# Kernel optimization log

Hardware: AMD Instinct MI355X
Metric: run time of the kernel (lower is better)

## Reference

```python
import jax, jax.numpy as jnp
import numpy as np
import math

N_NODES = 50000
N_EDGES = 800000
D_IN = 128
HID = 128  # layer dims: 128 -> 128 -> 64 -> 32


def _glorot(key, fan_in, fan_out):
    lim = math.sqrt(6.0 / (fan_in + fan_out))
    return jax.random.uniform(key, (fan_in, fan_out), jnp.float32, -lim, lim)


def setup_inputs() -> dict:
    key = jax.random.key(0)
    ks = jax.random.split(key, 9)
    x = jax.random.normal(ks[0], (N_NODES, D_IN), dtype=jnp.float32)
    edge_index = jax.random.randint(ks[1], (2, N_EDGES), 0, N_NODES, dtype=jnp.int64)
    edge_attr = jax.random.uniform(ks[2], (N_EDGES,), dtype=jnp.float32)
    return {
        "x": x,
        "edge_index": edge_index,
        "edge_attr": edge_attr,
        "W1": _glorot(ks[3], D_IN, HID),      "b1": jnp.zeros((HID,), jnp.float32),
        "W2": _glorot(ks[4], HID, HID // 2),  "b2": jnp.zeros((HID // 2,), jnp.float32),
        "W3": _glorot(ks[5], HID // 2, HID // 4), "b3": jnp.zeros((HID // 4,), jnp.float32),
    }


def _gcn_conv(h, W, b, src, dst, norm, n_nodes):
    # GCNConv: linear transform, then normalized scatter-add aggregation, then bias
    h = h @ W                                   # [N, F_out]
    msg = h[src] * norm[:, None]                # gather + scale, [E', F_out]
    out = jax.ops.segment_sum(msg, dst, num_segments=n_nodes)  # scatter-add
    return out + b


def reference(x, edge_index, edge_attr, W1, b1, W2, b2, W3, b3):
    n = x.shape[0]
    # add self-loops with weight 1.0 (PyG GCNConv default)
    loop = jnp.arange(n, dtype=edge_index.dtype)
    src = jnp.concatenate([edge_index[0], loop])
    dst = jnp.concatenate([edge_index[1], loop])
    w = jnp.concatenate([edge_attr, jnp.ones((n,), edge_attr.dtype)])
    # symmetric normalization: D^{-1/2} A_hat D^{-1/2}
    deg = jax.ops.segment_sum(w, dst, num_segments=n)
    dinv = jnp.where(deg > 0, jax.lax.rsqrt(jnp.maximum(deg, 1e-30)), 0.0)
    norm = dinv[src] * w * dinv[dst]            # [E + N]

    h = jax.nn.relu(_gcn_conv(x, W1, b1, src, dst, norm, n))
    # dropout is identity in eval mode
    h = jax.nn.relu(_gcn_conv(h, W2, b2, src, dst, norm, n))
    h = _gcn_conv(h, W3, b3, src, dst, norm, n)
    return h
```

## Files before the change

kernel.cpp:

```cpp
#include <hip/hip_runtime.h>
#include <hip/hip_bf16.h>

#define BLK 256
#define SCAT_NB 512
#define BIN_SHIFT 8

typedef unsigned short ushort_t;
typedef unsigned int uint_t;
typedef unsigned long long ull_t;
typedef __attribute__((ext_vector_type(8))) short bf16x8;
typedef __attribute__((ext_vector_type(4))) float f32x4;

static __device__ __forceinline__ float bf2f(ushort_t u) {
    return __uint_as_float((uint_t)u << 16);
}
static __device__ __forceinline__ ushort_t f2bf(float f) {
    __hip_bfloat16 h = __float2bfloat16(f);
    return *reinterpret_cast<ushort_t*>(&h);
}


__global__ __launch_bounds__(256) void k_pre(const int* __restrict__ eidx,
                                             int* __restrict__ bcnt,
                                             int nbins, int epb, int E,
                                             const float* __restrict__ x,
                                             ushort_t* __restrict__ xb, int n4,
                                             const float* __restrict__ W1, ushort_t* __restrict__ Wt1,
                                             const float* __restrict__ W2, ushort_t* __restrict__ Wt2,
                                             const float* __restrict__ W3, ushort_t* __restrict__ Wt3) {
    const int b = blockIdx.x;
    const int t = threadIdx.x;
    if (b < SCAT_NB) {
        __shared__ int h[256];
        h[t] = 0;
        __syncthreads();
        const int base = b * epb;
        const int lim  = min(base + epb, E);
        for (int e = base + t; e < lim; e += 256)
            atomicAdd(&h[eidx[E + e] >> BIN_SHIFT], 1);
        __syncthreads();
        if (t < nbins) bcnt[(size_t)t * SCAT_NB + b] = h[t];
    } else {
        int i = (b - SCAT_NB) * 256 + t;
        if (i < n4) {
            float4 v = ((const float4*)x)[i];
            ((ushort4*)xb)[i] = make_ushort4(f2bf(v.x), f2bf(v.y), f2bf(v.z), f2bf(v.w));
        } else {
            int j = i - n4;
            if (j < 128 * 128) {
                int r = j / 128, c = j % 128;
                Wt1[(size_t)c * 128 + r] = f2bf(W1[j]);
            } else if (j < 128 * 128 + 128 * 64) {
                j -= 128 * 128;
                int r = j / 64, c = j % 64;
                Wt2[(size_t)c * 128 + r] = f2bf(W2[j]);
            } else if (j < 128 * 128 + 128 * 64 + 64 * 32) {
                j -= 128 * 128 + 128 * 64;
                int r = j / 32, c = j % 32;
                Wt3[(size_t)c * 64 + r] = f2bf(W3[j]);
            }
        }
    }
}


__global__ __launch_bounds__(256) void k_scan1(const int* __restrict__ cnt,
                                               int* rowptr, int* bsum, int n) {
    __shared__ int tile[256];
    const int t = threadIdx.x;
    const int i = blockIdx.x * 256 + t;
    int v = (i < n) ? cnt[i] : 0;
    tile[t] = v;
    __syncthreads();
    for (int off = 1; off < 256; off <<= 1) {
        int x = (t >= off) ? tile[t - off] : 0;
        __syncthreads();
        tile[t] += x;
        __syncthreads();
    }
    if (i < n) rowptr[i] = tile[t] - v;
    if (t == 255) bsum[blockIdx.x] = tile[255];
}

__global__ __launch_bounds__(256) void k_scan2x(int* a, int n) {
    __shared__ int tile[256];
    __shared__ int carry_s;
    const int t = threadIdx.x;
    if (t == 0) carry_s = 0;
    __syncthreads();
    for (int base = 0; base < n; base += 256) {
        int i = base + t;
        int v = (i < n) ? a[i] : 0;
        tile[t] = v;
        __syncthreads();
        for (int off = 1; off < 256; off <<= 1) {
            int x = (t >= off) ? tile[t - off] : 0;
            __syncthreads();
            tile[t] += x;
            __syncthreads();
        }
        int carry = carry_s;
        if (i < n) a[i] = carry + tile[t] - v;
        __syncthreads();
        if (t == 255) carry_s = carry + tile[255];
        __syncthreads();
    }
}



__global__ __launch_bounds__(256) void k_bin_scatter(const int* __restrict__ eidx,
                                                     const float* __restrict__ ea,
                                                     const int* __restrict__ ebofs,
                                                     const int* __restrict__ bsumB,
                                                     int2* __restrict__ binned_sd,
                                                     float* __restrict__ binned_ea,
                                                     int nbins, int epb, int E) {
    __shared__ int h[256];
    __shared__ int lofs[256];
    const int t = threadIdx.x;
    h[t] = 0;
    if (t < nbins) {
        int idx = t * SCAT_NB + blockIdx.x;
        lofs[t] = ebofs[idx] + bsumB[idx >> 8];
    }
    __syncthreads();
    const int base = blockIdx.x * epb;
    const int lim  = min(base + epb, E);
    for (int e = base + t; e < lim; e += 256) {
        int s = eidx[e];
        int d = eidx[E + e];
        float w = ea[e];
        int bin = d >> BIN_SHIFT;
        int r = atomicAdd(&h[bin], 1);
        int pos = lofs[bin] + r;
        binned_sd[pos] = make_int2(s, d);
        binned_ea[pos] = w;
    }
}

__global__ __launch_bounds__(256) void k_bin_hist(const int2* __restrict__ binned_sd,
                                                  const float* __restrict__ binned_ea,
                                                  const int* __restrict__ ebofs,
                                                  const int* __restrict__ bsumB,
                                                  float* __restrict__ dinv,
                                                  float* __restrict__ selfn,
                                                  int* __restrict__ rowptr,
                                                  int nbins, int N, int E) {
    __shared__ ull_t hs[256];
    __shared__ int sc[256];
    const int t = threadIdx.x;
    const int b = blockIdx.x;
    hs[t] = 0ull;
    __syncthreads();
    const int i0 = b * SCAT_NB;
    const int start = ebofs[i0] + bsumB[i0 >> 8];
    int end = E;
    if (b + 1 < nbins) {
        int i1 = (b + 1) * SCAT_NB;
        end = ebofs[i1] + bsumB[i1 >> 8];
    }
    for (int i = start + t; i < end; i += 256) {
        int d = binned_sd[i].y;
        float w = binned_ea[i];
        atomicAdd(&hs[d & 255], (1ull << 40) | (ull_t)(w * 4294967296.0f));
    }
    __syncthreads();
    int v = (int)(hs[t] >> 40);
    sc[t] = v;
    __syncthreads();
    for (int off = 1; off < 256; off <<= 1) {
        int x = (t >= off) ? sc[t - off] : 0;
        __syncthreads();
        sc[t] += x;
        __syncthreads();
    }
    const int node = (b << BIN_SHIFT) + t;
    if (node < N) {
        ull_t s = hs[t];
        float dg = 1.0f + (float)(s & ((1ull << 40) - 1)) * (1.0f / 4294967296.0f);
        dinv[node]  = rsqrtf(dg);
        selfn[node] = 1.0f / dg;
        rowptr[node] = start + sc[t] - v;
    }
    if (b == 0 && t == 0) rowptr[N] = E;
}

__global__ __launch_bounds__(256) void k_bin_emit(const int2* __restrict__ binned_sd,
                                                  const float* __restrict__ binned_ea,
                                                  const int* __restrict__ ebofs,
                                                  const int* __restrict__ bsumB,
                                                  const int* __restrict__ rowptr,
                                                  const float* __restrict__ dinv,
                                                  int* __restrict__ csr_src,
                                                  float* __restrict__ csr_val,
                                                  int nbins, int E) {
    __shared__ int c2[256];
    const int t = threadIdx.x;
    const int b = blockIdx.x;
    c2[t] = 0;
    __syncthreads();
    const int i0 = b * SCAT_NB;
    const int start = ebofs[i0] + bsumB[i0 >> 8];
    int end = E;
    if (b + 1 < nbins) {
        int i1 = (b + 1) * SCAT_NB;
        end = ebofs[i1] + bsumB[i1 >> 8];
    }
    for (int i = start + t; i < end; i += 256) {
        int2 sd = binned_sd[i];
        float w = binned_ea[i];
        int r = atomicAdd(&c2[sd.y & 255], 1);
        int pos = rowptr[sd.y] + r;
        csr_src[pos] = sd.x;
        csr_val[pos] = dinv[sd.x] * w * dinv[sd.y];
    }
}


template <int FIN, int FOUT>
__global__ __launch_bounds__(256) void k_gemm_mfma(const ushort_t* __restrict__ A,
                                                   const ushort_t* __restrict__ Wt,
                                                   ushort_t* __restrict__ C, int n) {
    constexpr int NT = FOUT / 16;
    constexpr int NK = FIN / 32;
    const int wave = threadIdx.x >> 6;
    const int lane = threadIdx.x & 63;
    const int r0 = (blockIdx.x * 4 + wave) * 32;
    if (r0 >= n) return;

    const int l15 = lane & 15;
    const int kg  = lane >> 4;
    const int arow0 = min(r0 + l15, n - 1);
    const int arow1 = min(r0 + 16 + l15, n - 1);

    f32x4 acc0[NT], acc1[NT];
#pragma unroll
    for (int c = 0; c < NT; ++c) { acc0[c] = (f32x4)(0.0f); acc1[c] = (f32x4)(0.0f); }

    const ushort_t* Ap0 = A + (size_t)arow0 * FIN + kg * 8;
    const ushort_t* Ap1 = A + (size_t)arow1 * FIN + kg * 8;
    const ushort_t* Bp  = Wt + (size_t)l15 * FIN + kg * 8;

#pragma unroll 1
    for (int ks = 0; ks < NK; ++ks) {
        bf16x8 a0 = *(const bf16x8*)(Ap0 + ks * 32);
        bf16x8 a1 = *(const bf16x8*)(Ap1 + ks * 32);
#pragma unroll
        for (int c = 0; c < NT; ++c) {
            bf16x8 bfr = *(const bf16x8*)(Bp + (size_t)c * 16 * FIN + ks * 32);
            acc0[c] = __builtin_amdgcn_mfma_f32_16x16x32_bf16(a0, bfr, acc0[c], 0, 0, 0);
            acc1[c] = __builtin_amdgcn_mfma_f32_16x16x32_bf16(a1, bfr, acc1[c], 0, 0, 0);
        }
    }

#pragma unroll
    for (int g = 0; g < 2; ++g) {
        const int rbase = r0 + g * 16 + kg * 4;
#pragma unroll
        for (int c = 0; c < NT; ++c) {
#pragma unroll
            for (int j = 0; j < 4; ++j) {
                int row = rbase + j;
                float val = (g == 0) ? acc0[c][j] : acc1[c][j];
                if (row < n) C[(size_t)row * FOUT + c * 16 + l15] = f2bf(val);
            }
        }
    }
}


template <int FOUT, bool RELU, bool OBF16>
__global__ __launch_bounds__(256) void k_agg(const ushort_t* __restrict__ H,
                                             const float* __restrict__ selfn,
                                             const int* __restrict__ rowptr,
                                             const int* __restrict__ csr_src,
                                             const float* __restrict__ csr_val,
                                             const float* __restrict__ bias,
                                             void* __restrict__ outv, int n) {
    constexpr int LPN = FOUT / 2;
    constexpr int NPW = 64 / LPN;
    const int wave = threadIdx.x >> 6;
    const int lane = threadIdx.x & 63;
    const int sub  = lane / LPN;
    const int f2   = lane % LPN;
    const int node = (blockIdx.x * 4 + wave) * NPW + sub;
    if (node >= n) return;

    const ushort_t* __restrict__ Hf = H + 2 * f2;

    const float sn = selfn[node];
    ushort2 hv = *(const ushort2*)(Hf + (size_t)node * FOUT);
    float acc0 = sn * bf2f(hv.x);
    float acc1 = sn * bf2f(hv.y);

    const int e0 = rowptr[node], e1 = rowptr[node + 1];
    int e = e0;
    for (; e + 8 <= e1; e += 8) {
        int   s0 = csr_src[e+0], s1 = csr_src[e+1], s2 = csr_src[e+2], s3 = csr_src[e+3];
        int   s4 = csr_src[e+4], s5 = csr_src[e+5], s6 = csr_src[e+6], s7 = csr_src[e+7];
        float v0 = csr_val[e+0], v1 = csr_val[e+1], v2 = csr_val[e+2], v3 = csr_val[e+3];
        float v4 = csr_val[e+4], v5 = csr_val[e+5], v6 = csr_val[e+6], v7 = csr_val[e+7];
        ushort2 m0 = *(const ushort2*)(Hf + (size_t)s0 * FOUT);
        ushort2 m1 = *(const ushort2*)(Hf + (size_t)s1 * FOUT);
        ushort2 m2 = *(const ushort2*)(Hf + (size_t)s2 * FOUT);
        ushort2 m3 = *(const ushort2*)(Hf + (size_t)s3 * FOUT);
        ushort2 m4 = *(const ushort2*)(Hf + (size_t)s4 * FOUT);
        ushort2 m5 = *(const ushort2*)(Hf + (size_t)s5 * FOUT);
        ushort2 m6 = *(const ushort2*)(Hf + (size_t)s6 * FOUT);
        ushort2 m7 = *(const ushort2*)(Hf + (size_t)s7 * FOUT);
        acc0 += v0 * bf2f(m0.x); acc1 += v0 * bf2f(m0.y);
        acc0 += v1 * bf2f(m1.x); acc1 += v1 * bf2f(m1.y);
        acc0 += v2 * bf2f(m2.x); acc1 += v2 * bf2f(m2.y);
        acc0 += v3 * bf2f(m3.x); acc1 += v3 * bf2f(m3.y);
        acc0 += v4 * bf2f(m4.x); acc1 += v4 * bf2f(m4.y);
        acc0 += v5 * bf2f(m5.x); acc1 += v5 * bf2f(m5.y);
        acc0 += v6 * bf2f(m6.x); acc1 += v6 * bf2f(m6.y);
        acc0 += v7 * bf2f(m7.x); acc1 += v7 * bf2f(m7.y);
    }
    for (; e + 2 <= e1; e += 2) {
        int   s0 = csr_src[e+0], s1 = csr_src[e+1];
        float v0 = csr_val[e+0], v1 = csr_val[e+1];
        ushort2 m0 = *(const ushort2*)(Hf + (size_t)s0 * FOUT);
        ushort2 m1 = *(const ushort2*)(Hf + (size_t)s1 * FOUT);
        acc0 += v0 * bf2f(m0.x); acc1 += v0 * bf2f(m0.y);
        acc0 += v1 * bf2f(m1.x); acc1 += v1 * bf2f(m1.y);
    }
    if (e < e1) {
        int   s0 = csr_src[e];
        float v0 = csr_val[e];
        ushort2 m0 = *(const ushort2*)(Hf + (size_t)s0 * FOUT);
        acc0 += v0 * bf2f(m0.x); acc1 += v0 * bf2f(m0.y);
    }

    acc0 += bias[2 * f2];
    acc1 += bias[2 * f2 + 1];
    if (RELU) { acc0 = fmaxf(acc0, 0.f); acc1 = fmaxf(acc1, 0.f); }
    if (OBF16) {
        ushort2 o = make_ushort2(f2bf(acc0), f2bf(acc1));
        *(ushort2*)((ushort_t*)outv + (size_t)node * FOUT + 2 * f2) = o;
    } else {
        *(float2*)((float*)outv + (size_t)node * FOUT + 2 * f2) = make_float2(acc0, acc1);
    }
}


extern "C" void kernel_launch(void* const* d_in, const int* in_sizes, int n_in,
                              void* d_out, int out_size, void* d_ws, size_t ws_size,
                              hipStream_t stream) {
    const float* x    = (const float*)d_in[0];
    const int*   eidx = (const int*)d_in[1];
    const float* ea   = (const float*)d_in[2];
    const float* W1   = (const float*)d_in[3];
    const float* b1   = (const float*)d_in[4];
    const float* W2   = (const float*)d_in[5];
    const float* b2   = (const float*)d_in[6];
    const float* W3   = (const float*)d_in[7];
    const float* b3   = (const float*)d_in[8];

    const int N = in_sizes[0] / 128;
    const int E = in_sizes[2];

    const int nbins = (N + 255) >> BIN_SHIFT;
    const int epb   = (E + SCAT_NB - 1) / SCAT_NB;
    const int nbc   = nbins * SCAT_NB;
    const int gBC   = (nbc + BLK - 1) / BLK;

    char*  base = (char*)d_ws;
    size_t off  = 0;
    auto carve = [&](size_t nbytes) -> void* {
        void* p = base + off;
        off = (off + nbytes + 255) & ~(size_t)255;
        return p;
    };
    int*   bcnt      = (int*)  carve((size_t)nbc * 4);
    int*   ebofs     = (int*)  carve((size_t)nbc * 4);
    int*   bsumB     = (int*)  carve((size_t)512 * 4);
    int2*  binned_sd = (int2*) carve((size_t)E * 8);
    float* binned_ea = (float*)carve((size_t)E * 4);
    float* dinv      = (float*)carve((size_t)N * 4);
    float* selfn     = (float*)carve((size_t)N * 4);
    int*   rowptr    = (int*)  carve((size_t)(N + 1) * 4);
    int*   csr_src   = (int*)  carve((size_t)E * 4);
    float* csr_val   = (float*)carve((size_t)E * 4);
    ushort_t* bufA   = (ushort_t*)carve((size_t)N * 128 * 2);
    ushort_t* bufB   = (ushort_t*)carve((size_t)N * 128 * 2);
    ushort_t* Wt1    = (ushort_t*)carve((size_t)128 * 128 * 2);
    ushort_t* Wt2    = (ushort_t*)carve((size_t)64 * 128 * 2);
    ushort_t* Wt3    = (ushort_t*)carve((size_t)32 * 64 * 2);
    (void)ws_size;

    const int n4 = N * 128 / 4;
    const int gPre = SCAT_NB + (n4 + 128 * 128 + 128 * 64 + 64 * 32 + 255) / 256;
    const int gR = (N + 127) / 128;

    k_pre<<<gPre, BLK, 0, stream>>>(eidx, bcnt, nbins, epb, E,
                                    x, bufB, n4, W1, Wt1, W2, Wt2, W3, Wt3);
    k_scan1<<<gBC, BLK, 0, stream>>>(bcnt, ebofs, bsumB, nbc);
    k_scan2x<<<1, BLK, 0, stream>>>(bsumB, gBC);
    k_bin_scatter<<<SCAT_NB, BLK, 0, stream>>>(eidx, ea, ebofs, bsumB, binned_sd, binned_ea, nbins, epb, E);
    k_bin_hist<<<nbins, BLK, 0, stream>>>(binned_sd, binned_ea, ebofs, bsumB, dinv, selfn, rowptr, nbins, N, E);
    k_bin_emit<<<nbins, BLK, 0, stream>>>(binned_sd, binned_ea, ebofs, bsumB, rowptr, dinv,
                                          csr_src, csr_val, nbins, E);

    k_gemm_mfma<128, 128><<<gR, BLK, 0, stream>>>(bufB, Wt1, bufA, N);
    k_agg<128, true, true><<<(N + 3) / 4, BLK, 0, stream>>>(bufA, selfn, rowptr, csr_src, csr_val, b1, bufB, N);

    k_gemm_mfma<128, 64><<<gR, BLK, 0, stream>>>(bufB, Wt2, bufA, N);
    k_agg<64, true, true><<<(N + 7) / 8, BLK, 0, stream>>>(bufA, selfn, rowptr, csr_src, csr_val, b2, bufB, N);

    k_gemm_mfma<64, 32><<<gR, BLK, 0, stream>>>(bufB, Wt3, bufA, N);
    k_agg<32, false, false><<<(N + 15) / 16, BLK, 0, stream>>>(bufA, selfn, rowptr, csr_src, csr_val, b3, d_out, N);
}
```

Measured before the change: 156.8 us.

## Fuse CSR build into one cooperative kernel and widen aggregation to 4 features per lane

Merges the six graph-preprocessing kernels (histogram, two scans, bin scatter, bin histogram, CSR emit) into one cooperative kernel that separates phases with grid-wide syncs, removing launch gaps between them. It also changes the aggregation kernels so each lane handles four features with 8-byte gathers instead of two, which halves lanes per node and packs more nodes into each wave. The fused kernel runs every phase on only 512 blocks and pays for grid barriers. The wider gathers may reduce memory-level parallelism per node.

New measurement: 439.3 us. 2.8x slower.

```diff
diff --git a/kernel.cpp b/kernel.cpp
--- a/kernel.cpp
+++ b/kernel.cpp
@@ -1,5 +1,8 @@
 #include <hip/hip_runtime.h>
 #include <hip/hip_bf16.h>
+#include <hip/hip_cooperative_groups.h>
+
+namespace cg = cooperative_groups;
 
 #define BLK 256
 #define SCAT_NB 512
@@ -20,18 +23,27 @@
 }
 
 
-__global__ __launch_bounds__(256) void k_pre(const int* __restrict__ eidx,
-                                             int* __restrict__ bcnt,
-                                             int nbins, int epb, int E,
-                                             const float* __restrict__ x,
-                                             ushort_t* __restrict__ xb, int n4,
-                                             const float* __restrict__ W1, ushort_t* __restrict__ Wt1,
-                                             const float* __restrict__ W2, ushort_t* __restrict__ Wt2,
-                                             const float* __restrict__ W3, ushort_t* __restrict__ Wt3) {
+__global__ __launch_bounds__(256) void k_build(
+    const int* __restrict__ eidx, const float* __restrict__ ea,
+    int nbins, int epb, int E, int N,
+    const float* __restrict__ x, ushort_t* __restrict__ xb, int n4,
+    const float* __restrict__ W1, ushort_t* __restrict__ Wt1,
+    const float* __restrict__ W2, ushort_t* __restrict__ Wt2,
+    const float* __restrict__ W3, ushort_t* __restrict__ Wt3,
+    int* __restrict__ bcnt, int* __restrict__ ebofs, int* __restrict__ bsumB,
+    int2* __restrict__ binned_sd, float* __restrict__ binned_ea,
+    float* __restrict__ dinv, float* __restrict__ selfn, int* __restrict__ rowptr,
+    int* __restrict__ csr_src, float* __restrict__ csr_val)
+{
+    cg::grid_group grid = cg::this_grid();
+    __shared__ ull_t smem64[256];
+    __shared__ int   smemi[256];
     const int b = blockIdx.x;
     const int t = threadIdx.x;
-    if (b < SCAT_NB) {
-        __shared__ int h[256];
+    const int nb = gridDim.x;
+
+    {
+        int* h = smemi;
         h[t] = 0;
         __syncthreads();
         const int base = b * epb;
@@ -40,180 +52,143 @@
             atomicAdd(&h[eidx[E + e] >> BIN_SHIFT], 1);
         __syncthreads();
         if (t < nbins) bcnt[(size_t)t * SCAT_NB + b] = h[t];
-    } else {
-        int i = (b - SCAT_NB) * 256 + t;
-        if (i < n4) {
-            float4 v = ((const float4*)x)[i];
-            ((ushort4*)xb)[i] = make_ushort4(f2bf(v.x), f2bf(v.y), f2bf(v.z), f2bf(v.w));
-        } else {
-            int j = i - n4;
-            if (j < 128 * 128) {
-                int r = j / 128, c = j % 128;
-                Wt1[(size_t)c * 128 + r] = f2bf(W1[j]);
-            } else if (j < 128 * 128 + 128 * 64) {
-                j -= 128 * 128;
-                int r = j / 64, c = j % 64;
-                Wt2[(size_t)c * 128 + r] = f2bf(W2[j]);
-            } else if (j < 128 * 128 + 128 * 64 + 64 * 32) {
-                j -= 128 * 128 + 128 * 64;
-                int r = j / 32, c = j % 32;
-                Wt3[(size_t)c * 64 + r] = f2bf(W3[j]);
+        const int wtot = 128 * 128 + 128 * 64 + 64 * 32;
+        for (int i = b * 256 + t; i < n4 + wtot; i += nb * 256) {
+            if (i < n4) {
+                float4 v = ((const float4*)x)[i];
+                ((ushort4*)xb)[i] = make_ushort4(f2bf(v.x), f2bf(v.y), f2bf(v.z), f2bf(v.w));
+            } else {
+                int j = i - n4;
+                if (j < 128 * 128) { int r = j / 128, c = j % 128; Wt1[(size_t)c * 128 + r] = f2bf(W1[j]); }
+                else if (j < 128 * 128 + 128 * 64) { j -= 128 * 128; int r = j / 64, c = j % 64; Wt2[(size_t)c * 128 + r] = f2bf(W2[j]); }
+                else { j -= 128 * 128 + 128 * 64; int r = j / 32, c = j % 32; Wt3[(size_t)c * 64 + r] = f2bf(W3[j]); }
             }
         }
     }
-}
-
-
-__global__ __launch_bounds__(256) void k_scan1(const int* __restrict__ cnt,
-                                               int* rowptr, int* bsum, int n) {
-    __shared__ int tile[256];
-    const int t = threadIdx.x;
-    const int i = blockIdx.x * 256 + t;
-    int v = (i < n) ? cnt[i] : 0;
-    tile[t] = v;
-    __syncthreads();
-    for (int off = 1; off < 256; off <<= 1) {
-        int x = (t >= off) ? tile[t - off] : 0;
-        __syncthreads();
-        tile[t] += x;
-        __syncthreads();
-    }
-    if (i < n) rowptr[i] = tile[t] - v;
-    if (t == 255) bsum[blockIdx.x] = tile[255];
-}
-
-__global__ __launch_bounds__(256) void k_scan2x(int* a, int n) {
-    __shared__ int tile[256];
-    __shared__ int carry_s;
-    const int t = threadIdx.x;
-    if (t == 0) carry_s = 0;
-    __syncthreads();
-    for (int base = 0; base < n; base += 256) {
-        int i = base + t;
-        int v = (i < n) ? a[i] : 0;
-        tile[t] = v;
+    grid.sync();
+
+    const int nbc = nbins * SCAT_NB;
+    const int nchunk = (nbc + 255) / 256;
+    {
+        int* tile = smemi;
+        for (int c = b; c < nchunk; c += nb) {
+            int i = c * 256 + t;
+            int v = (i < nbc) ? bcnt[i] : 0;
+            tile[t] = v;
+            __syncthreads();
+            for (int off = 1; off < 256; off <<= 1) {
+                int xx = (t >= off) ? tile[t - off] : 0;
+                __syncthreads();
+                tile[t] += xx;
+                __syncthreads();
+            }
+            if (i < nbc) ebofs[i] = tile[t] - v;
+            if (t == 255) bsumB[c] = tile[255];
+            __syncthreads();
+        }
+    }
+    grid.sync();
+
+    if (b == 0) {
+        int* tile = smemi;
+        __shared__ int carry_s;
+        if (t == 0) carry_s = 0;
+        __syncthreads();
+        for (int base2 = 0; base2 < nchunk; base2 += 256) {
+            int i = base2 + t;
+            int v = (i < nchunk) ? bsumB[i] : 0;
+            tile[t] = v;
+            __syncthreads();
+            for (int off = 1; off < 256; off <<= 1) {
+                int xx = (t >= off) ? tile[t - off] : 0;
+                __syncthreads();
+                tile[t] += xx;
+                __syncthreads();
+            }
+            int carry = carry_s;
+            if (i < nchunk) bsumB[i] = carry + tile[t] - v;
+            __syncthreads();
+            if (t == 255) carry_s = carry + tile[255];
+            __syncthreads();
+        }
+    }
+    grid.sync();
+
+    {
+        int* h = smemi;
+        int* lofs = (int*)smem64;
+        h[t] = 0;
+        if (t < nbins) {
+            int idx = t * SCAT_NB + b;
+            lofs[t] = ebofs[idx] + bsumB[idx >> 8];
+        }
+        __syncthreads();
+        const int base = b * epb;
+        const int lim  = min(base + epb, E);
+        for (int e = base + t; e < lim; e += 256) {
+            int s = eidx[e];
+            int d = eidx[E + e];
+            float w = ea[e];
+            int bin = d >> BIN_SHIFT;
+            int r = atomicAdd(&h[bin], 1);
+            int pos = lofs[bin] + r;
+            binned_sd[pos] = make_int2(s, d);
+            binned_ea[pos] = w;
+        }
+    }
+    grid.sync();
+
+    if (b < nbins) {
+        ull_t* hs = smem64;
+        int* sc = smemi;
+        hs[t] = 0ull;
+        __syncthreads();
+        const int i0 = b * SCAT_NB;
+        const int start = ebofs[i0] + bsumB[i0 >> 8];
+        int end = E;
+        if (b + 1 < nbins) { int i1 = (b + 1) * SCAT_NB; end = ebofs[i1] + bsumB[i1 >> 8]; }
+        for (int i = start + t; i < end; i += 256) {
+            int d = binned_sd[i].y;
+            atomicAdd(&hs[d & 255], (1ull << 40) | (ull_t)(binned_ea[i] * 4294967296.0f));
+        }
+        __syncthreads();
+        int v = (int)(hs[t] >> 40);
+        sc[t] = v;
         __syncthreads();
         for (int off = 1; off < 256; off <<= 1) {
-            int x = (t >= off) ? tile[t - off] : 0;
-            __syncthreads();
-            tile[t] += x;
-            __syncthreads();
-        }
-        int carry = carry_s;
-        if (i < n) a[i] = carry + tile[t] - v;
-        __syncthreads();
-        if (t == 255) carry_s = carry + tile[255];
-        __syncthreads();
-    }
-}
-
-
-
-__global__ __launch_bounds__(256) void k_bin_scatter(const int* __restrict__ eidx,
-                                                     const float* __restrict__ ea,
-                                                     const int* __restrict__ ebofs,
-                                                     const int* __restrict__ bsumB,
-                                                     int2* __restrict__ binned_sd,
-                                                     float* __restrict__ binned_ea,
-                                                     int nbins, int epb, int E) {
-    __shared__ int h[256];
-    __shared__ int lofs[256];
-    const int t = threadIdx.x;
-    h[t] = 0;
-    if (t < nbins) {
-        int idx = t * SCAT_NB + blockIdx.x;
-        lofs[t] = ebofs[idx] + bsumB[idx >> 8];
-    }
-    __syncthreads();
-    const int base = blockIdx.x * epb;
-    const int lim  = min(base + epb, E);
-    for (int e = base + t; e < lim; e += 256) {
-        int s = eidx[e];
-        int d = eidx[E + e];
-        float w = ea[e];
-        int bin = d >> BIN_SHIFT;
-        int r = atomicAdd(&h[bin], 1);
-        int pos = lofs[bin] + r;
-        binned_sd[pos] = make_int2(s, d);
-        binned_ea[pos] = w;
-    }
-}
-
-__global__ __launch_bounds__(256) void k_bin_hist(const int2* __restrict__ binned_sd,
-                                                  const float* __restrict__ binned_ea,
-                                                  const int* __restrict__ ebofs,
-                                                  const int* __restrict__ bsumB,
-                                                  float* __restrict__ dinv,
-                                                  float* __restrict__ selfn,
-                                                  int* __restrict__ rowptr,
-                                                  int nbins, int N, int E) {
-    __shared__ ull_t hs[256];
-    __shared__ int sc[256];
-    const int t = threadIdx.x;
-    const int b = blockIdx.x;
-    hs[t] = 0ull;
-    __syncthreads();
-    const int i0 = b * SCAT_NB;
-    const int start = ebofs[i0] + bsumB[i0 >> 8];
-    int end = E;
-    if (b + 1 < nbins) {
-        int i1 = (b + 1) * SCAT_NB;
-        end = ebofs[i1] + bsumB[i1 >> 8];
-    }
-    for (int i = start + t; i < end; i += 256) {
-        int d = binned_sd[i].y;
-        float w = binned_ea[i];
-        atomicAdd(&hs[d & 255], (1ull << 40) | (ull_t)(w * 4294967296.0f));
-    }
-    __syncthreads();
-    int v = (int)(hs[t] >> 40);
-    sc[t] = v;
-    __syncthreads();
-    for (int off = 1; off < 256; off <<= 1) {
-        int x = (t >= off) ? sc[t - off] : 0;
-        __syncthreads();
-        sc[t] += x;
-        __syncthreads();
-    }
-    const int node = (b << BIN_SHIFT) + t;
-    if (node < N) {
-        ull_t s = hs[t];
-        float dg = 1.0f + (float)(s & ((1ull << 40) - 1)) * (1.0f / 4294967296.0f);
-        dinv[node]  = rsqrtf(dg);
-        selfn[node] = 1.0f / dg;
-        rowptr[node] = start + sc[t] - v;
-    }
-    if (b == 0 && t == 0) rowptr[N] = E;
-}
-
-__global__ __launch_bounds__(256) void k_bin_emit(const int2* __restrict__ binned_sd,
-                                                  const float* __restrict__ binned_ea,
-                                                  const int* __restrict__ ebofs,
-                                                  const int* __restrict__ bsumB,
-                                                  const int* __restrict__ rowptr,
-                                                  const float* __restrict__ dinv,
-                                                  int* __restrict__ csr_src,
-                                                  float* __restrict__ csr_val,
-                                                  int nbins, int E) {
-    __shared__ int c2[256];
-    const int t = threadIdx.x;
-    const int b = blockIdx.x;
-    c2[t] = 0;
-    __syncthreads();
-    const int i0 = b * SCAT_NB;
-    const int start = ebofs[i0] + bsumB[i0 >> 8];
-    int end = E;
-    if (b + 1 < nbins) {
-        int i1 = (b + 1) * SCAT_NB;
-        end = ebofs[i1] + bsumB[i1 >> 8];
-    }
-    for (int i = start + t; i < end; i += 256) {
-        int2 sd = binned_sd[i];
-        float w = binned_ea[i];
-        int r = atomicAdd(&c2[sd.y & 255], 1);
-        int pos = rowptr[sd.y] + r;
-        csr_src[pos] = sd.x;
-        csr_val[pos] = dinv[sd.x] * w * dinv[sd.y];
+            int xx = (t >= off) ? sc[t - off] : 0;
+            __syncthreads();
+            sc[t] += xx;
+            __syncthreads();
+        }
+        const int node = (b << BIN_SHIFT) + t;
+        if (node < N) {
+            ull_t s = hs[t];
+            float dg = 1.0f + (float)(s & ((1ull << 40) - 1)) * (1.0f / 4294967296.0f);
+            dinv[node]  = rsqrtf(dg);
+            selfn[node] = 1.0f / dg;
+            rowptr[node] = start + sc[t] - v;
+        }
+        if (b == 0 && t == 0) rowptr[N] = E;
+    }
+    grid.sync();
+
+    if (b < nbins) {
+        int* c2 = smemi;
+        c2[t] = 0;
+        __syncthreads();
+        const int i0 = b * SCAT_NB;
+        const int start = ebofs[i0] + bsumB[i0 >> 8];
+        int end = E;
+        if (b + 1 < nbins) { int i1 = (b + 1) * SCAT_NB; end = ebofs[i1] + bsumB[i1 >> 8]; }
+        for (int i = start + t; i < end; i += 256) {
+            int2 sd = binned_sd[i];
+            float w = binned_ea[i];
+            int r = atomicAdd(&c2[sd.y & 255], 1);
+            int pos = rowptr[sd.y] + r;
+            csr_src[pos] = sd.x;
+            csr_val[pos] = dinv[sd.x] * w * dinv[sd.y];
+        }
     }
 }
 
@@ -278,21 +253,23 @@
                                              const float* __restrict__ csr_val,
                                              const float* __restrict__ bias,
                                              void* __restrict__ outv, int n) {
-    constexpr int LPN = FOUT / 2;
+    constexpr int LPN = FOUT / 4;
     constexpr int NPW = 64 / LPN;
     const int wave = threadIdx.x >> 6;
     const int lane = threadIdx.x & 63;
     const int sub  = lane / LPN;
-    const int f2   = lane % LPN;
+    const int f4   = lane % LPN;
     const int node = (blockIdx.x * 4 + wave) * NPW + sub;
     if (node >= n) return;
 
-    const ushort_t* __restrict__ Hf = H + 2 * f2;
+    const ushort_t* __restrict__ Hf = H + 4 * f4;
 
     const float sn = selfn[node];
-    ushort2 hv = *(const ushort2*)(Hf + (size_t)node * FOUT);
-    float acc0 = sn * bf2f(hv.x);
-    float acc1 = sn * bf2f(hv.y);
+    ushort4 hv = *(const ushort4*)(Hf + (size_t)node * FOUT);
+    float a0 = sn * bf2f(hv.x);
+    float a1 = sn * bf2f(hv.y);
+    float a2 = sn * bf2f(hv.z);
+    float a3 = sn * bf2f(hv.w);
 
     const int e0 = rowptr[node], e1 = rowptr[node + 1];
     int e = e0;
@@ -301,46 +278,49 @@
         int   s4 = csr_src[e+4], s5 = csr_src[e+5], s6 = csr_src[e+6], s7 = csr_src[e+7];
         float v0 = csr_val[e+0], v1 = csr_val[e+1], v2 = csr_val[e+2], v3 = csr_val[e+3];
         float v4 = csr_val[e+4], v5 = csr_val[e+5], v6 = csr_val[e+6], v7 = csr_val[e+7];
-        ushort2 m0 = *(const ushort2*)(Hf + (size_t)s0 * FOUT);
-        ushort2 m1 = *(const ushort2*)(Hf + (size_t)s1 * FOUT);
-        ushort2 m2 = *(const ushort2*)(Hf + (size_t)s2 * FOUT);
-        ushort2 m3 = *(const ushort2*)(Hf + (size_t)s3 * FOUT);
-        ushort2 m4 = *(const ushort2*)(Hf + (size_t)s4 * FOUT);
-        ushort2 m5 = *(const ushort2*)(Hf + (size_t)s5 * FOUT);
-        ushort2 m6 = *(const ushort2*)(Hf + (size_t)s6 * FOUT);
-        ushort2 m7 = *(const ushort2*)(Hf + (size_t)s7 * FOUT);
-        acc0 += v0 * bf2f(m0.x); acc1 += v0 * bf2f(m0.y);
-        acc0 += v1 * bf2f(m1.x); acc1 += v1 * bf2f(m1.y);
-        acc0 += v2 * bf2f(m2.x); acc1 += v2 * bf2f(m2.y);
-        acc0 += v3 * bf2f(m3.x); acc1 += v3 * bf2f(m3.y);
-        acc0 += v4 * bf2f(m4.x); acc1 += v4 * bf2f(m4.y);
-        acc0 += v5 * bf2f(m5.x); acc1 += v5 * bf2f(m5.y);
-        acc0 += v6 * bf2f(m6.x); acc1 += v6 * bf2f(m6.y);
-        acc0 += v7 * bf2f(m7.x); acc1 += v7 * bf2f(m7.y);
+        ushort4 m0 = *(const ushort4*)(Hf + (size_t)s0 * FOUT);
+        ushort4 m1 = *(const ushort4*)(Hf + (size_t)s1 * FOUT);
+        ushort4 m2 = *(const ushort4*)(Hf + (size_t)s2 * FOUT);
+        ushort4 m3 = *(const ushort4*)(Hf + (size_t)s3 * FOUT);
+        ushort4 m4 = *(const ushort4*)(Hf + (size_t)s4 * FOUT);
+        ushort4 m5 = *(const ushort4*)(Hf + (size_t)s5 * FOUT);
+        ushort4 m6 = *(const ushort4*)(Hf + (size_t)s6 * FOUT);
+        ushort4 m7 = *(const ushort4*)(Hf + (size_t)s7 * FOUT);
+        a0 += v0 * bf2f(m0.x); a1 += v0 * bf2f(m0.y); a2 += v0 * bf2f(m0.z); a3 += v0 * bf2f(m0.w);
+        a0 += v1 * bf2f(m1.x); a1 += v1 * bf2f(m1.y); a2 += v1 * bf2f(m1.z); a3 += v1 * bf2f(m1.w);
+        a0 += v2 * bf2f(m2.x); a1 += v2 * bf2f(m2.y); a2 += v2 * bf2f(m2.z); a3 += v2 * bf2f(m2.w);
+        a0 += v3 * bf2f(m3.x); a1 += v3 * bf2f(m3.y); a2 += v3 * bf2f(m3.z); a3 += v3 * bf2f(m3.w);
+        a0 += v4 * bf2f(m4.x); a1 += v4 * bf2f(m4.y); a2 += v4 * bf2f(m4.z); a3 += v4 * bf2f(m4.w);
+        a0 += v5 * bf2f(m5.x); a1 += v5 * bf2f(m5.y); a2 += v5 * bf2f(m5.z); a3 += v5 * bf2f(m5.w);
+        a0 += v6 * bf2f(m6.x); a1 += v6 * bf2f(m6.y); a2 += v6 * bf2f(m6.z); a3 += v6 * bf2f(m6.w);
+        a0 += v7 * bf2f(m7.x); a1 += v7 * bf2f(m7.y); a2 += v7 * bf2f(m7.z); a3 += v7 * bf2f(m7.w);
     }
     for (; e + 2 <= e1; e += 2) {
         int   s0 = csr_src[e+0], s1 = csr_src[e+1];
         float v0 = csr_val[e+0], v1 = csr_val[e+1];
-        ushort2 m0 = *(const ushort2*)(Hf + (size_t)s0 * FOUT);
-        ushort2 m1 = *(const ushort2*)(Hf + (size_t)s1 * FOUT);
-        acc0 += v0 * bf2f(m0.x); acc1 += v0 * bf2f(m0.y);
-        acc0 += v1 * bf2f(m1.x); acc1 += v1 * bf2f(m1.y);
+        ushort4 m0 = *(const ushort4*)(Hf + (size_t)s0 * FOUT);
+        ushort4 m1 = *(const ushort4*)(Hf + (size_t)s1 * FOUT);
+        a0 += v0 * bf2f(m0.x); a1 += v0 * bf2f(m0.y); a2 += v0 * bf2f(m0.z); a3 += v0 * bf2f(m0.w);
+        a0 += v1 * bf2f(m1.x); a1 += v1 * bf2f(m1.y); a2 += v1 * bf2f(m1.z); a3 += v1 * bf2f(m1.w);
     }
     if (e < e1) {
         int   s0 = csr_src[e];
         float v0 = csr_val[e];
-        ushort2 m0 = *(const ushort2*)(Hf + (size_t)s0 * FOUT);
-        acc0 += v0 * bf2f(m0.x); acc1 += v0 * bf2f(m0.y);
-    }
-
-    acc0 += bias[2 * f2];
-    acc1 += bias[2 * f2 + 1];
-    if (RELU) { acc0 = fmaxf(acc0, 0.f); acc1 = fmaxf(acc1, 0.f); }
+        ushort4 m0 = *(const ushort4*)(Hf + (size_t)s0 * FOUT);
+        a0 += v0 * bf2f(m0.x); a1 += v0 * bf2f(m0.y); a2 += v0 * bf2f(m0.z); a3 += v0 * bf2f(m0.w);
+    }
+
+    float4 bv = *(const float4*)(bias + 4 * f4);
+    a0 += bv.x; a1 += bv.y; a2 += bv.z; a3 += bv.w;
+    if (RELU) {
+        a0 = fmaxf(a0, 0.f); a1 = fmaxf(a1, 0.f);
+        a2 = fmaxf(a2, 0.f); a3 = fmaxf(a3, 0.f);
+    }
     if (OBF16) {
-        ushort2 o = make_ushort2(f2bf(acc0), f2bf(acc1));
-        *(ushort2*)((ushort_t*)outv + (size_t)node * FOUT + 2 * f2) = o;
+        ushort4 o = make_ushort4(f2bf(a0), f2bf(a1), f2bf(a2), f2bf(a3));
+        *(ushort4*)((ushort_t*)outv + (size_t)node * FOUT + 4 * f4) = o;
     } else {
-        *(float2*)((float*)outv + (size_t)node * FOUT + 2 * f2) = make_float2(acc0, acc1);
+        *(float4*)((float*)outv + (size_t)node * FOUT + 4 * f4) = make_float4(a0, a1, a2, a3);
     }
 }
 
@@ -361,10 +341,9 @@
     const int N = in_sizes[0] / 128;
     const int E = in_sizes[2];
 
-    const int nbins = (N + 255) >> BIN_SHIFT;
-    const int epb   = (E + SCAT_NB - 1) / SCAT_NB;
-    const int nbc   = nbins * SCAT_NB;
-    const int gBC   = (nbc + BLK - 1) / BLK;
+    int nbins = (N + 255) >> BIN_SHIFT;
+    int epb   = (E + SCAT_NB - 1) / SCAT_NB;
+    const int nbc = nbins * SCAT_NB;
 
     char*  base = (char*)d_ws;
     size_t off  = 0;
@@ -390,25 +369,31 @@
     ushort_t* Wt3    = (ushort_t*)carve((size_t)32 * 64 * 2);
     (void)ws_size;
 
-    const int n4 = N * 128 / 4;
-    const int gPre = SCAT_NB + (n4 + 128 * 128 + 128 * 64 + 64 * 32 + 255) / 256;
+    int n4 = N * 128 / 4;
     const int gR = (N + 127) / 128;
 
-    k_pre<<<gPre, BLK, 0, stream>>>(eidx, bcnt, nbins, epb, E,
-                                    x, bufB, n4, W1, Wt1, W2, Wt2, W3, Wt3);
-    k_scan1<<<gBC, BLK, 0, stream>>>(bcnt, ebofs, bsumB, nbc);
-    k_scan2x<<<1, BLK, 0, stream>>>(bsumB, gBC);
-    k_bin_scatter<<<SCAT_NB, BLK, 0, stream>>>(eidx, ea, ebofs, bsumB, binned_sd, binned_ea, nbins, epb, E);
-    k_bin_hist<<<nbins, BLK, 0, stream>>>(binned_sd, binned_ea, ebofs, bsumB, dinv, selfn, rowptr, nbins, N, E);
-    k_bin_emit<<<nbins, BLK, 0, stream>>>(binned_sd, binned_ea, ebofs, bsumB, rowptr, dinv,
-                                          csr_src, csr_val, nbins, E);
+    {
+        ushort_t* xb = bufB;
+        int Nv = N, Ev = E;
+        void* args[] = {
+            (void*)&eidx, (void*)&ea, (void*)&nbins, (void*)&epb, (void*)&Ev, (void*)&Nv,
+            (void*)&x, (void*)&xb, (void*)&n4,
+            (void*)&W1, (void*)&Wt1, (void*)&W2, (void*)&Wt2, (void*)&W3, (void*)&Wt3,
+            (void*)&bcnt, (void*)&ebofs, (void*)&bsumB,
+            (void*)&binned_sd, (void*)&binned_ea,
+            (void*)&dinv, (void*)&selfn, (void*)&rowptr,
+            (void*)&csr_src, (void*)&csr_val
+        };
+        hipLaunchCooperativeKernel((const void*)k_build, dim3(SCAT_NB), dim3(BLK),
+                                   args, 0, stream);
+    }
 
     k_gemm_mfma<128, 128><<<gR, BLK, 0, stream>>>(bufB, Wt1, bufA, N);
-    k_agg<128, true, true><<<(N + 3) / 4, BLK, 0, stream>>>(bufA, selfn, rowptr, csr_src, csr_val, b1, bufB, N);
+    k_agg<128, true, true><<<(N + 7) / 8, BLK, 0, stream>>>(bufA, selfn, rowptr, csr_src, csr_val, b1, bufB, N);
 
     k_gemm_mfma<128, 64><<<gR, BLK, 0, stream>>>(bufB, Wt2, bufA, N);
-    k_agg<64, true, true><<<(N + 7) / 8, BLK, 0, stream>>>(bufA, selfn, rowptr, csr_src, csr_val, b2, bufB, N);
+    k_agg<64, true, true><<<(N + 15) / 16, BLK, 0, stream>>>(bufA, selfn, rowptr, csr_src, csr_val, b2, bufB, N);
 
     k_gemm_mfma<64, 32><<<gR, BLK, 0, stream>>>(bufB, Wt3, bufA, N);
-    k_agg<32, false, false><<<(N + 15) / 16, BLK, 0, stream>>>(bufA, selfn, rowptr, csr_src, csr_val, b3, d_out, N);
-}
+    k_agg<32, false, false><<<(N + 31) / 32, BLK, 0, stream>>>(bufA, selfn, rowptr, csr_src, csr_val, b3, d_out, N);
+}
```
